# Performance work log

Measured on AMD Instinct MI355X. Metric: run time of the kernel, lower is better.

## Reference

```python
import jax, jax.numpy as jnp
import numpy as np

B, N, M = 32, 65536, 64
IMG = 640.0
POS_THR, NEG_THR = 0.5, 0.4
ALPHA, GAMMA = 0.25, 2.0
BBOX_W = 2.0
EPS = 1e-6


def setup_inputs() -> dict:
    key = jax.random.key(0)
    k1, k2, k3, k4, k5 = jax.random.split(key, 5)
    # predictions: cx, cy in [0, IMG], w, h in [8, 72], obj logit ~ N(0,1)
    cxcy = jax.random.uniform(k1, (B, N, 2), jnp.float32) * IMG
    wh = jax.random.uniform(k2, (B, N, 2), jnp.float32) * 64.0 + 8.0
    obj = jax.random.normal(k3, (B, N, 1), jnp.float32)
    predictions = jnp.concatenate([cxcy, wh, obj], axis=-1)  # [B, N, 5]
    # ground-truth boxes in xyxy, centers in [0, IMG], sizes in [10, 100]
    gcxcy = jax.random.uniform(k4, (B, M, 2), jnp.float32) * IMG
    gwh = jax.random.uniform(k5, (B, M, 2), jnp.float32) * 90.0 + 10.0
    gt_boxes = jnp.concatenate([gcxcy - gwh / 2, gcxcy + gwh / 2], axis=-1)  # [B, M, 4]
    return {"predictions": predictions, "gt_boxes": gt_boxes}


def _focal(logits, targets):
    # stable BCE-with-logits, then focal modulation
    bce = jnp.maximum(logits, 0.0) - logits * targets + jnp.log1p(jnp.exp(-jnp.abs(logits)))
    p = jax.nn.sigmoid(logits)
    p_t = jnp.where(targets == 1.0, p, 1.0 - p)
    alpha_t = jnp.where(targets == 1.0, ALPHA, 1.0 - ALPHA)
    return alpha_t * (1.0 - p_t) ** GAMMA * bce


def _pairwise_iou(pb, gb):
    # pb: [N,4] xyxy, gb: [M,4] xyxy -> [N,M]
    x1 = jnp.maximum(pb[:, None, 0], gb[None, :, 0])
    y1 = jnp.maximum(pb[:, None, 1], gb[None, :, 1])
    x2 = jnp.minimum(pb[:, None, 2], gb[None, :, 2])
    y2 = jnp.minimum(pb[:, None, 3], gb[None, :, 3])
    inter = jnp.clip(x2 - x1, 0.0) * jnp.clip(y2 - y1, 0.0)
    area_p = (pb[:, 2] - pb[:, 0]) * (pb[:, 3] - pb[:, 1])
    area_g = (gb[:, 2] - gb[:, 0]) * (gb[:, 3] - gb[:, 1])
    union = area_p[:, None] + area_g[None, :] - inter
    return inter / jnp.clip(union, EPS)


def _giou_term(pb, gb):
    # elementwise 1 - GIoU; pb, gb: [N,4]
    x1 = jnp.maximum(pb[:, 0], gb[:, 0]); y1 = jnp.maximum(pb[:, 1], gb[:, 1])
    x2 = jnp.minimum(pb[:, 2], gb[:, 2]); y2 = jnp.minimum(pb[:, 3], gb[:, 3])
    inter = jnp.clip(x2 - x1, 0.0) * jnp.clip(y2 - y1, 0.0)
    area_p = (pb[:, 2] - pb[:, 0]) * (pb[:, 3] - pb[:, 1])
    area_g = (gb[:, 2] - gb[:, 0]) * (gb[:, 3] - gb[:, 1])
    union = area_p + area_g - inter
    iou = inter / jnp.clip(union, EPS)
    ex1 = jnp.minimum(pb[:, 0], gb[:, 0]); ey1 = jnp.minimum(pb[:, 1], gb[:, 1])
    ex2 = jnp.maximum(pb[:, 2], gb[:, 2]); ey2 = jnp.maximum(pb[:, 3], gb[:, 3])
    enc = (ex2 - ex1) * (ey2 - ey1)
    giou = iou - (enc - union) / jnp.clip(enc, EPS)
    return 1.0 - giou


def _per_image(pred, gt):
    # pred: [N,5] (cx,cy,w,h,obj), gt: [M,4] xyxy
    cx, cy, w, h = pred[:, 0], pred[:, 1], pred[:, 2], pred[:, 3]
    pb = jnp.stack([cx - w / 2, cy - h / 2, cx + w / 2, cy + h / 2], axis=1)  # decode to xyxy
    obj = pred[:, 4]
    ious = _pairwise_iou(pb, gt)  # [N, M]
    best_pred_per_gt = ious.max(axis=0)              # [M]
    best_pred_idx = jnp.argmax(ious, axis=0)         # [M]
    best_gt_per_pred = ious.max(axis=1)              # [N]
    best_gt_idx = jnp.argmax(ious, axis=1)           # [N]
    # force-match each GT's best anchor if its IoU > 0.1 (scatter-max)
    pos_scatter = jnp.zeros((pred.shape[0],), jnp.int32).at[best_pred_idx].max(
        (best_pred_per_gt > 0.1).astype(jnp.int32))
    pos = (pos_scatter > 0) | (best_gt_per_pred > POS_THR)
    neg = best_gt_per_pred < NEG_THR
    valid = pos | neg
    t = pos.astype(jnp.float32)
    fl = _focal(obj, t)
    vcnt = valid.sum().astype(jnp.float32)
    cls_loss = jnp.where(vcnt > 0, (fl * valid).sum() / jnp.maximum(vcnt, 1.0), 0.0)
    matched = gt[best_gt_idx]                        # [N,4]
    gterm = _giou_term(pb, matched)                  # [N]
    pcnt = pos.sum().astype(jnp.float32)
    reg_loss = jnp.where(pcnt > 0, (gterm * pos).sum() / jnp.maximum(pcnt, 1.0), 0.0)
    return cls_loss, reg_loss, pos.sum()


def reference(predictions, gt_boxes):
    cls_b, reg_b, npos_b = jax.vmap(_per_image)(predictions, gt_boxes)
    num_pos = jnp.maximum(npos_b.sum(), 1).astype(jnp.float32)
    bsz = jnp.float32(predictions.shape[0])
    total_cls = cls_b.sum() / bsz
    total_reg = reg_b.sum() / num_pos * bsz
    return total_cls + BBOX_W * total_reg
```

## Files before the change

### kernel.cpp

```cpp
#include <hip/hip_runtime.h>

#define NB 32
#define NPRED 65536
#define NGT 64
#define BLK 256
#define SLICES 64
#define PPT 4
#define NCB 128
#define CBIN_SCALE 0.2f

#define POS_THR 0.5f
#define NEG_THR 0.4f
#define SCAT_THR 0.1f
#define EPSF 1e-6f


__device__ __forceinline__ int cbin(float x) {
    int bi = (int)(x * CBIN_SCALE);
    return max(0, min(NCB - 1, bi));
}

__device__ __forceinline__ float focal_shared(float l, bool pos) {
    float e  = expf(-fabsf(l));
    float lg = log1pf(e);
    float rp = 1.f / (1.f + e);
    float p  = (l >= 0.f) ? rp : (1.f - rp);
    if (pos) { float q = 1.f - p; return 0.25f * q * q * ((fmaxf(l, 0.f) - l) + lg); }
    return 0.75f * p * p * (fmaxf(l, 0.f) + lg);
}

__device__ __forceinline__ float giou_term(float px1, float py1, float px2, float py2,
                                           float gx1, float gy1, float gx2, float gy2) {
    float x1 = fmaxf(px1, gx1), y1 = fmaxf(py1, gy1);
    float x2 = fminf(px2, gx2), y2 = fminf(py2, gy2);
    float dx = fmaxf(__fsub_rn(x2, x1), 0.f);
    float dy = fmaxf(__fsub_rn(y2, y1), 0.f);
    float inter = __fmul_rn(dx, dy);
    float ap = __fmul_rn(__fsub_rn(px2, px1), __fsub_rn(py2, py1));
    float ag = __fmul_rn(__fsub_rn(gx2, gx1), __fsub_rn(gy2, gy1));
    float uni = __fsub_rn(__fadd_rn(ap, ag), inter);
    float iou = __fdiv_rn(inter, fmaxf(uni, EPSF));
    float ex1 = fminf(px1, gx1), ey1 = fminf(py1, gy1);
    float ex2 = fmaxf(px2, gx2), ey2 = fmaxf(py2, gy2);
    float enc = __fmul_rn(__fsub_rn(ex2, ex1), __fsub_rn(ey2, ey1));
    float giou = __fsub_rn(iou, __fdiv_rn(__fsub_rn(enc, uni), fmaxf(enc, EPSF)));
    return __fsub_rn(1.f, giou);
}


__global__ __launch_bounds__(BLK) void passA(
    const float* __restrict__ pred, const float* __restrict__ gt,
    unsigned long long* __restrict__ keys,
    double* __restrict__ S_fl, double* __restrict__ S_gt,
    int* __restrict__ vcnt, int* __restrict__ pcnt)
{
    const int b = blockIdx.y;
    const int slice = blockIdx.x;
    const int tid = threadIdx.x;
    const int lane = tid & 63;
    const int wv = tid >> 6;

    __shared__ float sgx1[NGT + 1], sgy1[NGT + 1], sgx2[NGT + 1], sgy2[NGT + 1], sgar[NGT + 1];
    __shared__ unsigned long long skey[NGT];
    __shared__ unsigned long long cums[4][NCB];
    __shared__ float rfl[BLK / 64], rgt[BLK / 64];
    __shared__ int rvp[BLK / 64];

    const unsigned base_n = (unsigned)(slice * (BLK * PPT));
    const float4* src4 = (const float4*)(pred + (size_t)b * NPRED * 5 + (size_t)base_n * 5)
                         + (size_t)tid * 5;
    float4 q0 = src4[0], q1 = src4[1], q2 = src4[2], q3 = src4[3], q4 = src4[4];

    const float4* gtb = (const float4*)(gt + (size_t)b * NGT * 4);
    float4 gmine;
    if (tid < NGT) gmine = gtb[tid];
    ((unsigned long long*)cums)[tid] = 0ULL;
    ((unsigned long long*)cums)[tid + BLK] = 0ULL;
    if (tid < NGT) {
        sgx1[tid] = gmine.x; sgy1[tid] = gmine.y;
        sgx2[tid] = gmine.z; sgy2[tid] = gmine.w;
        sgar[tid] = __fmul_rn(__fsub_rn(gmine.z, gmine.x), __fsub_rn(gmine.w, gmine.y));
        skey[tid] = 0ULL;
    } else if (tid == NGT) {
        sgx1[NGT] = 0.f; sgy1[NGT] = 0.f; sgx2[NGT] = 0.f; sgy2[NGT] = 0.f; sgar[NGT] = 0.f;
    }
    __syncthreads();

    if (tid < NGT) {
        unsigned long long bit = 1ULL << tid;
        atomicOr(&cums[0][cbin(gmine.x)], bit);
        atomicOr(&cums[1][cbin(gmine.z)], bit);
        atomicOr(&cums[2][cbin(gmine.y)], bit);
        atomicOr(&cums[3][cbin(gmine.w)], bit);
    }
    __syncthreads();

    {
        unsigned long long v0 = cums[wv][2 * lane];
        unsigned long long v1 = cums[wv][2 * lane + 1];
        unsigned long long v = v0 | v1;
        if ((wv & 1) == 0) {
            #pragma unroll
            for (int off = 1; off < 64; off <<= 1) {
                unsigned long long t = __shfl_up(v, off);
                if (lane >= off) v |= t;
            }
            unsigned long long prev = __shfl_up(v, 1);
            if (lane == 0) prev = 0ULL;
            cums[wv][2 * lane]     = prev | v0;
            cums[wv][2 * lane + 1] = v;
        } else {
            #pragma unroll
            for (int off = 1; off < 64; off <<= 1) {
                unsigned long long t = __shfl_down(v, off);
                if (lane + off < 64) v |= t;
            }
            unsigned long long nxt = __shfl_down(v, 1);
            if (lane == 63) nxt = 0ULL;
            cums[wv][2 * lane]     = v;
            cums[wv][2 * lane + 1] = v1 | nxt;
        }
    }
    __syncthreads();

    const float cxa[PPT] = {q0.x, q1.y, q2.z, q3.w};
    const float cya[PPT] = {q0.y, q1.z, q2.w, q4.x};
    const float wa [PPT] = {q0.z, q1.w, q3.x, q4.y};
    const float ha [PPT] = {q0.w, q2.x, q3.y, q4.z};
    const float oba[PPT] = {q1.x, q2.y, q3.z, q4.w};

    float acc_fl = 0.f, acc_gt = 0.f;
    int acc_vp = 0;

    #pragma unroll
    for (int i = 0; i < PPT; ++i) {
        const float px1 = __fsub_rn(cxa[i], __fmul_rn(wa[i], 0.5f));
        const float py1 = __fsub_rn(cya[i], __fmul_rn(ha[i], 0.5f));
        const float px2 = __fadd_rn(cxa[i], __fmul_rn(wa[i], 0.5f));
        const float py2 = __fadd_rn(cya[i], __fmul_rn(ha[i], 0.5f));
        const float area_p = __fmul_rn(__fsub_rn(px2, px1), __fsub_rn(py2, py1));

        unsigned long long m = (cums[1][cbin(px1)] & cums[0][cbin(px2)])
                             & (cums[3][cbin(py1)] & cums[2][cbin(py2)]);

        const unsigned n = base_n + (unsigned)(PPT * tid + i);
        const unsigned long long nkey = (unsigned long long)(~n);

        float best_iou = 0.f;
        int best_j = 0;

        int j0 = NGT, j1 = NGT;
        if (m) { j0 = __ffsll(m) - 1; m &= m - 1; }
        if (m) { j1 = __ffsll(m) - 1; m &= m - 1; }
        {
            float ax1 = sgx1[j0], ay1 = sgy1[j0], ax2 = sgx2[j0], ay2 = sgy2[j0], aga = sgar[j0];
            float bx1 = sgx1[j1], by1 = sgy1[j1], bx2 = sgx2[j1], by2 = sgy2[j1], agb = sgar[j1];
            float x1 = fmaxf(px1, ax1), y1 = fmaxf(py1, ay1);
            float x2 = fminf(px2, ax2), y2 = fminf(py2, ay2);
            float dx = fmaxf(__fsub_rn(x2, x1), 0.f);
            float dy = fmaxf(__fsub_rn(y2, y1), 0.f);
            float inter = __fmul_rn(dx, dy);
            float uni = __fsub_rn(__fadd_rn(area_p, aga), inter);
            float iou = __fdiv_rn(inter, fmaxf(uni, EPSF));
            iou = (inter > 0.f) ? iou : 0.f;
            if (iou > best_iou) { best_iou = iou; best_j = j0; }
            if (iou > SCAT_THR)
                atomicMax(&skey[j0], (((unsigned long long)__float_as_uint(iou)) << 32) | nkey);

            float X1 = fmaxf(px1, bx1), Y1 = fmaxf(py1, by1);
            float X2 = fminf(px2, bx2), Y2 = fminf(py2, by2);
            float dX = fmaxf(__fsub_rn(X2, X1), 0.f);
            float dY = fmaxf(__fsub_rn(Y2, Y1), 0.f);
            float interB = __fmul_rn(dX, dY);
            float uniB = __fsub_rn(__fadd_rn(area_p, agb), interB);
            float iouB = __fdiv_rn(interB, fmaxf(uniB, EPSF));
            iouB = (interB > 0.f) ? iouB : 0.f;
            if (iouB > best_iou) { best_iou = iouB; best_j = j1; }
            if (iouB > SCAT_THR)
                atomicMax(&skey[j1], (((unsigned long long)__float_as_uint(iouB)) << 32) | nkey);
        }

        while (m) {
            int ja = __ffsll(m) - 1; m &= m - 1;
            int jb = -1;
            if (m) { jb = __ffsll(m) - 1; m &= m - 1; }
            int jbc = (jb >= 0) ? jb : NGT;
            float ax1 = sgx1[ja], ay1 = sgy1[ja], ax2 = sgx2[ja], ay2 = sgy2[ja], aga = sgar[ja];
            float bx1 = sgx1[jbc], by1 = sgy1[jbc], bx2 = sgx2[jbc], by2 = sgy2[jbc], agb = sgar[jbc];
            {
                float x1 = fmaxf(px1, ax1), y1 = fmaxf(py1, ay1);
                float x2 = fminf(px2, ax2), y2 = fminf(py2, ay2);
                float dx = fmaxf(__fsub_rn(x2, x1), 0.f);
                float dy = fmaxf(__fsub_rn(y2, y1), 0.f);
                float inter = __fmul_rn(dx, dy);
                if (inter > 0.f) {
                    float uni = __fsub_rn(__fadd_rn(area_p, aga), inter);
                    float iou = __fdiv_rn(inter, fmaxf(uni, EPSF));
                    if (iou > best_iou) { best_iou = iou; best_j = ja; }
                    if (iou > SCAT_THR)
                        atomicMax(&skey[ja], (((unsigned long long)__float_as_uint(iou)) << 32) | nkey);
                }
            }
            if (jb >= 0) {
                float x1 = fmaxf(px1, bx1), y1 = fmaxf(py1, by1);
                float x2 = fminf(px2, bx2), y2 = fminf(py2, by2);
                float dx = fmaxf(__fsub_rn(x2, x1), 0.f);
                float dy = fmaxf(__fsub_rn(y2, y1), 0.f);
                float inter = __fmul_rn(dx, dy);
                if (inter > 0.f) {
                    float uni = __fsub_rn(__fadd_rn(area_p, agb), inter);
                    float iou = __fdiv_rn(inter, fmaxf(uni, EPSF));
                    if (iou > best_iou) { best_iou = iou; best_j = jb; }
                    if (iou > SCAT_THR)
                        atomicMax(&skey[jb], (((unsigned long long)__float_as_uint(iou)) << 32) | nkey);
                }
            }
        }

        const bool pos0   = best_iou > POS_THR;
        const bool negf   = best_iou < NEG_THR;
        const bool valid0 = pos0 || negf;
        if (valid0) acc_fl += focal_shared(oba[i], pos0);
        if (pos0) {
            acc_gt += giou_term(px1, py1, px2, py2,
                                sgx1[best_j], sgy1[best_j], sgx2[best_j], sgy2[best_j]);
        }
        acc_vp += (valid0 ? 1 : 0) | (pos0 ? 0x10000 : 0);
    }

    for (int off = 32; off; off >>= 1) {
        acc_fl += __shfl_down(acc_fl, off);
        acc_gt += __shfl_down(acc_gt, off);
        acc_vp += __shfl_down(acc_vp, off);
    }
    if (lane == 0) { rfl[wv] = acc_fl; rgt[wv] = acc_gt; rvp[wv] = acc_vp; }
    __syncthreads();
    if (tid == 0) {
        float sfl = 0.f, sgt2 = 0.f; int svp = 0;
        #pragma unroll
        for (int i = 0; i < BLK / 64; ++i) { sfl += rfl[i]; sgt2 += rgt[i]; svp += rvp[i]; }
        atomicAdd(&S_fl[b], (double)sfl);
        atomicAdd(&S_gt[b], (double)sgt2);
        atomicAdd(&vcnt[b], svp & 0xFFFF);
        atomicAdd(&pcnt[b], svp >> 16);
    }
    if (tid < NGT) {
        unsigned long long k = skey[tid];
        if (k) atomicMax(&keys[b * NGT + tid], k);
    }
}


__global__ __launch_bounds__(64) void passBC(
    const float* __restrict__ pred, const float* __restrict__ gt,
    const unsigned long long* __restrict__ keys,
    const double* __restrict__ S_fl, const double* __restrict__ S_gt,
    const int* __restrict__ vcnt, const int* __restrict__ pcnt,
    float* __restrict__ cls_b, float* __restrict__ reg_b, int* __restrict__ npos_b,
    unsigned* __restrict__ done, float* __restrict__ out)
{
    const int b = blockIdx.x;
    const int lane = threadIdx.x;

    __shared__ float4 sgt[NGT];
    __shared__ unsigned cn_list[NGT];

    const float4* gtb = (const float4*)(gt + (size_t)b * NGT * 4);
    float4 gj = gtb[lane];
    sgt[lane] = gj;

    unsigned long long key = keys[b * NGT + lane];
    float miou = __uint_as_float((unsigned)(key >> 32));
    unsigned n = ~((unsigned)(key & 0xFFFFFFFFULL));
    bool qual = miou > SCAT_THR;

    bool unique = qual;
    for (int j2 = 0; j2 < NGT; ++j2) {
        unsigned bn = __shfl(n, j2);
        int bq = __shfl((int)qual, j2);
        if (bq && j2 < lane && bn == n) unique = false;
    }
    unsigned long long mask = __ballot(unique ? 1 : 0);
    int NC = __popcll(mask);
    int slot = __popcll(mask & ((1ULL << lane) - 1ULL));
    if (unique) cn_list[slot] = n;
    __syncthreads();

    float cx = 0.f, cy = 0.f, w = 0.f, h = 0.f, obj = 0.f;
    if (lane < NC) {
        const float* p = pred + (size_t)b * NPRED * 5 + (size_t)cn_list[lane] * 5;
        cx = p[0]; cy = p[1]; w = p[2]; h = p[3]; obj = p[4];
    }
    float px1 = __fsub_rn(cx, __fmul_rn(w, 0.5f));
    float py1 = __fsub_rn(cy, __fmul_rn(h, 0.5f));
    float px2 = __fadd_rn(cx, __fmul_rn(w, 0.5f));
    float py2 = __fadd_rn(cy, __fmul_rn(h, 0.5f));
    float area_p = __fmul_rn(__fsub_rn(px2, px1), __fsub_rn(py2, py1));

    float bv = 0.f; int bj = 0;
    #pragma unroll 4
    for (int j = 0; j < NGT; ++j) {
        float4 g = sgt[j];
        float x1 = fmaxf(px1, g.x), y1 = fmaxf(py1, g.y);
        float x2 = fminf(px2, g.z), y2 = fminf(py2, g.w);
        float dx = fmaxf(__fsub_rn(x2, x1), 0.f);
        float dy = fmaxf(__fsub_rn(y2, y1), 0.f);
        float inter = __fmul_rn(dx, dy);
        if (inter > 0.f) {
            float ag = __fmul_rn(__fsub_rn(g.z, g.x), __fsub_rn(g.w, g.y));
            float uni = __fsub_rn(__fadd_rn(area_p, ag), inter);
            float iou = __fdiv_rn(inter, fmaxf(uni, EPSF));
            if (iou > bv) { bv = iou; bj = j; }
        }
    }

    double add_fl = 0.0, add_gt = 0.0;
    int add_v = 0, add_p = 0;
    if (lane < NC && !(bv > POS_THR)) {
        bool was_neg = bv < NEG_THR;
        float f1 = focal_shared(obj, true);
        float f0 = focal_shared(obj, false);
        add_fl = (double)f1 - (was_neg ? (double)f0 : 0.0);
        add_v = was_neg ? 0 : 1;
        add_p = 1;
        float4 gb = sgt[bj];
        add_gt = (double)giou_term(px1, py1, px2, py2, gb.x, gb.y, gb.z, gb.w);
    }

    for (int off = 32; off; off >>= 1) {
        add_fl += __shfl_down(add_fl, off);
        add_gt += __shfl_down(add_gt, off);
        add_v  += __shfl_down(add_v, off);
        add_p  += __shfl_down(add_p, off);
    }

    if (lane == 0) {
        double sfl = S_fl[b] + add_fl;
        double sgt2 = S_gt[b] + add_gt;
        int v = vcnt[b] + add_v;
        int pc = pcnt[b] + add_p;
        cls_b[b] = (v > 0) ? (float)(sfl / (double)(v > 1 ? v : 1)) : 0.f;
        reg_b[b] = (pc > 0) ? (float)(sgt2 / (double)(pc > 1 ? pc : 1)) : 0.f;
        npos_b[b] = pc;
    }

    __threadfence();
    unsigned t = 0;
    if (lane == 0) t = atomicAdd(done, 1u);
    t = __shfl(t, 0);
    if (t == NB - 1) {
        __threadfence();
        volatile float* vc = cls_b;
        volatile float* vr = reg_b;
        volatile int*   vn = npos_b;
        float cv = (lane < NB) ? vc[lane] : 0.f;
        float rv = (lane < NB) ? vr[lane] : 0.f;
        int   nv = (lane < NB) ? vn[lane] : 0;
        for (int off = 32; off; off >>= 1) {
            cv += __shfl_down(cv, off);
            rv += __shfl_down(rv, off);
            nv += __shfl_down(nv, off);
        }
        if (lane == 0) {
            float num_pos = fmaxf((float)nv, 1.f);
            out[0] = cv / (float)NB + 2.0f * (rv / num_pos * (float)NB);
        }
    }
}


extern "C" void kernel_launch(void* const* d_in, const int* in_sizes, int n_in,
                              void* d_out, int out_size, void* d_ws, size_t ws_size,
                              hipStream_t stream) {
    const float* pred = (const float*)d_in[0];
    const float* gt   = (const float*)d_in[1];
    float* out = (float*)d_out;

    char* ws = (char*)d_ws;
    unsigned long long* keys = (unsigned long long*)(ws + 0);
    double* S_fl   = (double*)(ws + 16384);
    double* S_gt   = (double*)(ws + 16640);
    int* vcnt      = (int*)(ws + 16896);
    int* pcnt      = (int*)(ws + 17024);
    float* cls_b   = (float*)(ws + 17152);
    float* reg_b   = (float*)(ws + 17280);
    int* npos_b    = (int*)(ws + 17408);
    unsigned* done = (unsigned*)(ws + 17536);

    hipMemsetAsync(d_ws, 0, 17664, stream);

    dim3 gridA(SLICES, NB);
    passA<<<gridA, BLK, 0, stream>>>(pred, gt, keys, S_fl, S_gt, vcnt, pcnt);
    passBC<<<NB, 64, 0, stream>>>(pred, gt, keys, S_fl, S_gt, vcnt, pcnt,
                                  cls_b, reg_b, npos_b, done, out);
}
```

Before: 119.4 us.

## Replace global atomics and memset with per-slice partials reduced in single block

passA now writes each block's partial sums and per-GT keys into dedicated per-slice slots instead of issuing double atomicAdds and 64-bit atomicMax. The memset is dropped, and the 32-block passBC with its done-counter final reduction becomes one 1024-thread block. Each wave handles two images, reduces the 64 slice partials, and does the final sum in shared memory. This removes atomic contention and the memset launch. In exchange the workspace is larger, with about 1 MB of keys to read back, and the final stage runs in a single block.

After: 154.2 us. 1.29x slower.

```diff
diff --git a/kernel.cpp b/kernel.cpp
--- a/kernel.cpp
+++ b/kernel.cpp
@@ -50,9 +50,8 @@
 
 __global__ __launch_bounds__(BLK) void passA(
     const float* __restrict__ pred, const float* __restrict__ gt,
-    unsigned long long* __restrict__ keys,
-    double* __restrict__ S_fl, double* __restrict__ S_gt,
-    int* __restrict__ vcnt, int* __restrict__ pcnt)
+    unsigned long long* __restrict__ keysP,
+    float4* __restrict__ partS)
 {
     const int b = blockIdx.y;
     const int slice = blockIdx.x;
@@ -239,123 +238,132 @@
         float sfl = 0.f, sgt2 = 0.f; int svp = 0;
         #pragma unroll
         for (int i = 0; i < BLK / 64; ++i) { sfl += rfl[i]; sgt2 += rgt[i]; svp += rvp[i]; }
-        atomicAdd(&S_fl[b], (double)sfl);
-        atomicAdd(&S_gt[b], (double)sgt2);
-        atomicAdd(&vcnt[b], svp & 0xFFFF);
-        atomicAdd(&pcnt[b], svp >> 16);
+        partS[b * SLICES + slice] = make_float4(sfl, sgt2, __int_as_float(svp), 0.f);
     }
     if (tid < NGT) {
-        unsigned long long k = skey[tid];
-        if (k) atomicMax(&keys[b * NGT + tid], k);
-    }
-}
-
-
-__global__ __launch_bounds__(64) void passBC(
+        keysP[((size_t)(b * NGT + tid)) * SLICES + slice] = skey[tid];
+    }
+}
+
+
+__global__ __launch_bounds__(1024) void passB(
     const float* __restrict__ pred, const float* __restrict__ gt,
-    const unsigned long long* __restrict__ keys,
-    const double* __restrict__ S_fl, const double* __restrict__ S_gt,
-    const int* __restrict__ vcnt, const int* __restrict__ pcnt,
-    float* __restrict__ cls_b, float* __restrict__ reg_b, int* __restrict__ npos_b,
-    unsigned* __restrict__ done, float* __restrict__ out)
+    const unsigned long long* __restrict__ keysP,
+    const float4* __restrict__ partS,
+    float* __restrict__ out)
 {
-    const int b = blockIdx.x;
-    const int lane = threadIdx.x;
-
-    __shared__ float4 sgt[NGT];
-    __shared__ unsigned cn_list[NGT];
-
-    const float4* gtb = (const float4*)(gt + (size_t)b * NGT * 4);
-    float4 gj = gtb[lane];
-    sgt[lane] = gj;
-
-    unsigned long long key = keys[b * NGT + lane];
-    float miou = __uint_as_float((unsigned)(key >> 32));
-    unsigned n = ~((unsigned)(key & 0xFFFFFFFFULL));
-    bool qual = miou > SCAT_THR;
-
-    bool unique = qual;
-    for (int j2 = 0; j2 < NGT; ++j2) {
-        unsigned bn = __shfl(n, j2);
-        int bq = __shfl((int)qual, j2);
-        if (bq && j2 < lane && bn == n) unique = false;
-    }
-    unsigned long long mask = __ballot(unique ? 1 : 0);
-    int NC = __popcll(mask);
-    int slot = __popcll(mask & ((1ULL << lane) - 1ULL));
-    if (unique) cn_list[slot] = n;
-    __syncthreads();
-
-    float cx = 0.f, cy = 0.f, w = 0.f, h = 0.f, obj = 0.f;
-    if (lane < NC) {
-        const float* p = pred + (size_t)b * NPRED * 5 + (size_t)cn_list[lane] * 5;
-        cx = p[0]; cy = p[1]; w = p[2]; h = p[3]; obj = p[4];
-    }
-    float px1 = __fsub_rn(cx, __fmul_rn(w, 0.5f));
-    float py1 = __fsub_rn(cy, __fmul_rn(h, 0.5f));
-    float px2 = __fadd_rn(cx, __fmul_rn(w, 0.5f));
-    float py2 = __fadd_rn(cy, __fmul_rn(h, 0.5f));
-    float area_p = __fmul_rn(__fsub_rn(px2, px1), __fsub_rn(py2, py1));
-
-    float bv = 0.f; int bj = 0;
-    #pragma unroll 4
-    for (int j = 0; j < NGT; ++j) {
-        float4 g = sgt[j];
-        float x1 = fmaxf(px1, g.x), y1 = fmaxf(py1, g.y);
-        float x2 = fminf(px2, g.z), y2 = fminf(py2, g.w);
-        float dx = fmaxf(__fsub_rn(x2, x1), 0.f);
-        float dy = fmaxf(__fsub_rn(y2, y1), 0.f);
-        float inter = __fmul_rn(dx, dy);
-        if (inter > 0.f) {
-            float ag = __fmul_rn(__fsub_rn(g.z, g.x), __fsub_rn(g.w, g.y));
-            float uni = __fsub_rn(__fadd_rn(area_p, ag), inter);
-            float iou = __fdiv_rn(inter, fmaxf(uni, EPSF));
-            if (iou > bv) { bv = iou; bj = j; }
-        }
-    }
-
-    double add_fl = 0.0, add_gt = 0.0;
-    int add_v = 0, add_p = 0;
-    if (lane < NC && !(bv > POS_THR)) {
-        bool was_neg = bv < NEG_THR;
-        float f1 = focal_shared(obj, true);
-        float f0 = focal_shared(obj, false);
-        add_fl = (double)f1 - (was_neg ? (double)f0 : 0.0);
-        add_v = was_neg ? 0 : 1;
-        add_p = 1;
-        float4 gb = sgt[bj];
-        add_gt = (double)giou_term(px1, py1, px2, py2, gb.x, gb.y, gb.z, gb.w);
-    }
-
-    for (int off = 32; off; off >>= 1) {
-        add_fl += __shfl_down(add_fl, off);
-        add_gt += __shfl_down(add_gt, off);
-        add_v  += __shfl_down(add_v, off);
-        add_p  += __shfl_down(add_p, off);
-    }
-
-    if (lane == 0) {
-        double sfl = S_fl[b] + add_fl;
-        double sgt2 = S_gt[b] + add_gt;
-        int v = vcnt[b] + add_v;
-        int pc = pcnt[b] + add_p;
-        cls_b[b] = (v > 0) ? (float)(sfl / (double)(v > 1 ? v : 1)) : 0.f;
-        reg_b[b] = (pc > 0) ? (float)(sgt2 / (double)(pc > 1 ? pc : 1)) : 0.f;
-        npos_b[b] = pc;
-    }
-
-    __threadfence();
-    unsigned t = 0;
-    if (lane == 0) t = atomicAdd(done, 1u);
-    t = __shfl(t, 0);
-    if (t == NB - 1) {
-        __threadfence();
-        volatile float* vc = cls_b;
-        volatile float* vr = reg_b;
-        volatile int*   vn = npos_b;
-        float cv = (lane < NB) ? vc[lane] : 0.f;
-        float rv = (lane < NB) ? vr[lane] : 0.f;
-        int   nv = (lane < NB) ? vn[lane] : 0;
+    const int tid = threadIdx.x;
+    const int lane = tid & 63;
+    const int wv = tid >> 6;
+
+    __shared__ float4 sgt[16][NGT];
+    __shared__ unsigned cn_list[16][NGT];
+    __shared__ float clsL[NB], regL[NB];
+    __shared__ int npL[NB];
+
+    #pragma unroll
+    for (int r = 0; r < 2; ++r) {
+        const int b = r * 16 + wv;
+
+        const float4* gtb = (const float4*)(gt + (size_t)b * NGT * 4);
+        float4 gj = gtb[lane];
+        sgt[wv][lane] = gj;
+
+        const unsigned long long* kp = keysP + ((size_t)(b * NGT + lane)) * SLICES;
+        const ulonglong2* kp2 = (const ulonglong2*)kp;
+        unsigned long long key = 0ULL;
+        #pragma unroll
+        for (int s = 0; s < SLICES / 2; ++s) {
+            ulonglong2 kk = kp2[s];
+            key = (kk.x > key) ? kk.x : key;
+            key = (kk.y > key) ? kk.y : key;
+        }
+
+        float miou = __uint_as_float((unsigned)(key >> 32));
+        unsigned n = ~((unsigned)(key & 0xFFFFFFFFULL));
+        bool qual = miou > SCAT_THR;
+
+        bool unique = qual;
+        for (int j2 = 0; j2 < NGT; ++j2) {
+            unsigned bn = __shfl(n, j2);
+            int bq = __shfl((int)qual, j2);
+            if (bq && j2 < lane && bn == n) unique = false;
+        }
+        unsigned long long mask = __ballot(unique ? 1 : 0);
+        int NC = __popcll(mask);
+        int slot = __popcll(mask & ((1ULL << lane) - 1ULL));
+        if (unique) cn_list[wv][slot] = n;
+
+        float cx = 0.f, cy = 0.f, w = 0.f, h = 0.f, obj = 0.f;
+        if (lane < NC) {
+            const float* p = pred + (size_t)b * NPRED * 5 + (size_t)cn_list[wv][lane] * 5;
+            cx = p[0]; cy = p[1]; w = p[2]; h = p[3]; obj = p[4];
+        }
+        float px1 = __fsub_rn(cx, __fmul_rn(w, 0.5f));
+        float py1 = __fsub_rn(cy, __fmul_rn(h, 0.5f));
+        float px2 = __fadd_rn(cx, __fmul_rn(w, 0.5f));
+        float py2 = __fadd_rn(cy, __fmul_rn(h, 0.5f));
+        float area_p = __fmul_rn(__fsub_rn(px2, px1), __fsub_rn(py2, py1));
+
+        float bv = 0.f; int bj = 0;
+        #pragma unroll 4
+        for (int j = 0; j < NGT; ++j) {
+            float4 g = sgt[wv][j];
+            float x1 = fmaxf(px1, g.x), y1 = fmaxf(py1, g.y);
+            float x2 = fminf(px2, g.z), y2 = fminf(py2, g.w);
+            float dx = fmaxf(__fsub_rn(x2, x1), 0.f);
+            float dy = fmaxf(__fsub_rn(y2, y1), 0.f);
+            float inter = __fmul_rn(dx, dy);
+            if (inter > 0.f) {
+                float ag = __fmul_rn(__fsub_rn(g.z, g.x), __fsub_rn(g.w, g.y));
+                float uni = __fsub_rn(__fadd_rn(area_p, ag), inter);
+                float iou = __fdiv_rn(inter, fmaxf(uni, EPSF));
+                if (iou > bv) { bv = iou; bj = j; }
+            }
+        }
+
+        double add_fl = 0.0, add_gt = 0.0;
+        int add_v = 0, add_p = 0;
+        if (lane < NC && !(bv > POS_THR)) {
+            bool was_neg = bv < NEG_THR;
+            float f1 = focal_shared(obj, true);
+            float f0 = focal_shared(obj, false);
+            add_fl = (double)f1 - (was_neg ? (double)f0 : 0.0);
+            add_v = was_neg ? 0 : 1;
+            add_p = 1;
+            float4 gb = sgt[wv][bj];
+            add_gt = (double)giou_term(px1, py1, px2, py2, gb.x, gb.y, gb.z, gb.w);
+        }
+
+        float4 ps = partS[b * SLICES + lane];
+        double sfl = (double)ps.x;
+        double sgt2 = (double)ps.y;
+        int vpk = __float_as_int(ps.z);
+        int sv = vpk & 0xFFFF;
+        int sp = vpk >> 16;
+
+        sfl += add_fl; sgt2 += add_gt; sv += add_v; sp += add_p;
+
+        for (int off = 32; off; off >>= 1) {
+            sfl  += __shfl_down(sfl, off);
+            sgt2 += __shfl_down(sgt2, off);
+            sv   += __shfl_down(sv, off);
+            sp   += __shfl_down(sp, off);
+        }
+
+        if (lane == 0) {
+            clsL[b] = (sv > 0) ? (float)(sfl / (double)(sv > 1 ? sv : 1)) : 0.f;
+            regL[b] = (sp > 0) ? (float)(sgt2 / (double)(sp > 1 ? sp : 1)) : 0.f;
+            npL[b] = sp;
+        }
+    }
+
+    __syncthreads();
+
+    if (wv == 0) {
+        float cv = (lane < NB) ? clsL[lane] : 0.f;
+        float rv = (lane < NB) ? regL[lane] : 0.f;
+        int   nv = (lane < NB) ? npL[lane] : 0;
         for (int off = 32; off; off >>= 1) {
             cv += __shfl_down(cv, off);
             rv += __shfl_down(rv, off);
@@ -377,20 +385,10 @@
     float* out = (float*)d_out;
 
     char* ws = (char*)d_ws;
-    unsigned long long* keys = (unsigned long long*)(ws + 0);
-    double* S_fl   = (double*)(ws + 16384);
-    double* S_gt   = (double*)(ws + 16640);
-    int* vcnt      = (int*)(ws + 16896);
-    int* pcnt      = (int*)(ws + 17024);
-    float* cls_b   = (float*)(ws + 17152);
-    float* reg_b   = (float*)(ws + 17280);
-    int* npos_b    = (int*)(ws + 17408);
-    unsigned* done = (unsigned*)(ws + 17536);
-
-    hipMemsetAsync(d_ws, 0, 17664, stream);
+    unsigned long long* keysP = (unsigned long long*)(ws + 0);
+    float4* partS = (float4*)(ws + (size_t)NB * NGT * SLICES * 8);
 
     dim3 gridA(SLICES, NB);
-    passA<<<gridA, BLK, 0, stream>>>(pred, gt, keys, S_fl, S_gt, vcnt, pcnt);
-    passBC<<<NB, 64, 0, stream>>>(pred, gt, keys, S_fl, S_gt, vcnt, pcnt,
-                                  cls_b, reg_b, npos_b, done, out);
-}
+    passA<<<gridA, BLK, 0, stream>>>(pred, gt, keysP, partS);
+    passB<<<1, 1024, 0, stream>>>(pred, gt, keysP, partS, out);
+}
```

## Replace global atomics and memset with per-slice partials reduced in second pass

Applied to the files above, without the earlier changes.

Each passA block now writes its partial sums and per-GT max keys to dedicated per-slice slots instead of issuing double/int atomicAdd and 64-bit atomicMax to shared per-image counters. passB reduces the 64 slice partials per image with a max loop and a wave reduction. The done counter is reset inside passA, which removes the hipMemsetAsync launch. This removes atomic contention and one extra stream operation, at the cost of a larger workspace and extra reads in passB. Partial sums are now kept in float per slice rather than accumulated in double.

After: 114.4 us (median of 2 runs). 4.1% less time.

```diff
diff --git a/kernel.cpp b/kernel.cpp
--- a/kernel.cpp
+++ b/kernel.cpp
@@ -50,15 +50,17 @@
 
 __global__ __launch_bounds__(BLK) void passA(
     const float* __restrict__ pred, const float* __restrict__ gt,
-    unsigned long long* __restrict__ keys,
-    double* __restrict__ S_fl, double* __restrict__ S_gt,
-    int* __restrict__ vcnt, int* __restrict__ pcnt)
+    unsigned long long* __restrict__ keysP,
+    float4* __restrict__ partS,
+    unsigned* __restrict__ done)
 {
     const int b = blockIdx.y;
     const int slice = blockIdx.x;
     const int tid = threadIdx.x;
     const int lane = tid & 63;
     const int wv = tid >> 6;
+
+    if (b == 0 && slice == 0 && tid == 0) *done = 0u;
 
     __shared__ float sgx1[NGT + 1], sgy1[NGT + 1], sgx2[NGT + 1], sgy2[NGT + 1], sgar[NGT + 1];
     __shared__ unsigned long long skey[NGT];
@@ -239,23 +241,18 @@
         float sfl = 0.f, sgt2 = 0.f; int svp = 0;
         #pragma unroll
         for (int i = 0; i < BLK / 64; ++i) { sfl += rfl[i]; sgt2 += rgt[i]; svp += rvp[i]; }
-        atomicAdd(&S_fl[b], (double)sfl);
-        atomicAdd(&S_gt[b], (double)sgt2);
-        atomicAdd(&vcnt[b], svp & 0xFFFF);
-        atomicAdd(&pcnt[b], svp >> 16);
+        partS[b * SLICES + slice] = make_float4(sfl, sgt2, __int_as_float(svp), 0.f);
     }
     if (tid < NGT) {
-        unsigned long long k = skey[tid];
-        if (k) atomicMax(&keys[b * NGT + tid], k);
-    }
-}
-
-
-__global__ __launch_bounds__(64) void passBC(
+        keysP[((size_t)b * SLICES + slice) * NGT + tid] = skey[tid];
+    }
+}
+
+
+__global__ __launch_bounds__(64) void passB(
     const float* __restrict__ pred, const float* __restrict__ gt,
-    const unsigned long long* __restrict__ keys,
-    const double* __restrict__ S_fl, const double* __restrict__ S_gt,
-    const int* __restrict__ vcnt, const int* __restrict__ pcnt,
+    const unsigned long long* __restrict__ keysP,
+    const float4* __restrict__ partS,
     float* __restrict__ cls_b, float* __restrict__ reg_b, int* __restrict__ npos_b,
     unsigned* __restrict__ done, float* __restrict__ out)
 {
@@ -269,7 +266,14 @@
     float4 gj = gtb[lane];
     sgt[lane] = gj;
 
-    unsigned long long key = keys[b * NGT + lane];
+    const unsigned long long* kp = keysP + (size_t)b * SLICES * NGT + lane;
+    unsigned long long key = 0ULL;
+    #pragma unroll 16
+    for (int s = 0; s < SLICES; ++s) {
+        unsigned long long k = kp[(size_t)s * NGT];
+        key = (k > key) ? k : key;
+    }
+
     float miou = __uint_as_float((unsigned)(key >> 32));
     unsigned n = ~((unsigned)(key & 0xFFFFFFFFULL));
     bool qual = miou > SCAT_THR;
@@ -327,21 +331,24 @@
         add_gt = (double)giou_term(px1, py1, px2, py2, gb.x, gb.y, gb.z, gb.w);
     }
 
+    float4 ps = partS[b * SLICES + lane];
+    double sfl = (double)ps.x + add_fl;
+    double sgt2 = (double)ps.y + add_gt;
+    int vpk = __float_as_int(ps.z);
+    int sv = (vpk & 0xFFFF) + add_v;
+    int sp = (vpk >> 16) + add_p;
+
     for (int off = 32; off; off >>= 1) {
-        add_fl += __shfl_down(add_fl, off);
-        add_gt += __shfl_down(add_gt, off);
-        add_v  += __shfl_down(add_v, off);
-        add_p  += __shfl_down(add_p, off);
+        sfl  += __shfl_down(sfl, off);
+        sgt2 += __shfl_down(sgt2, off);
+        sv   += __shfl_down(sv, off);
+        sp   += __shfl_down(sp, off);
     }
 
     if (lane == 0) {
-        double sfl = S_fl[b] + add_fl;
-        double sgt2 = S_gt[b] + add_gt;
-        int v = vcnt[b] + add_v;
-        int pc = pcnt[b] + add_p;
-        cls_b[b] = (v > 0) ? (float)(sfl / (double)(v > 1 ? v : 1)) : 0.f;
-        reg_b[b] = (pc > 0) ? (float)(sgt2 / (double)(pc > 1 ? pc : 1)) : 0.f;
-        npos_b[b] = pc;
+        cls_b[b] = (sv > 0) ? (float)(sfl / (double)(sv > 1 ? sv : 1)) : 0.f;
+        reg_b[b] = (sp > 0) ? (float)(sgt2 / (double)(sp > 1 ? sp : 1)) : 0.f;
+        npos_b[b] = sp;
     }
 
     __threadfence();
@@ -377,20 +384,16 @@
     float* out = (float*)d_out;
 
     char* ws = (char*)d_ws;
-    unsigned long long* keys = (unsigned long long*)(ws + 0);
-    double* S_fl   = (double*)(ws + 16384);
-    double* S_gt   = (double*)(ws + 16640);
-    int* vcnt      = (int*)(ws + 16896);
-    int* pcnt      = (int*)(ws + 17024);
-    float* cls_b   = (float*)(ws + 17152);
-    float* reg_b   = (float*)(ws + 17280);
-    int* npos_b    = (int*)(ws + 17408);
-    unsigned* done = (unsigned*)(ws + 17536);
-
-    hipMemsetAsync(d_ws, 0, 17664, stream);
+    unsigned long long* keysP = (unsigned long long*)(ws + 0);
+    float4* partS = (float4*)(ws + (size_t)NB * SLICES * NGT * 8);
+    char* tail = ws + (size_t)NB * SLICES * NGT * 8 + (size_t)NB * SLICES * 16;
+    float* cls_b   = (float*)(tail);
+    float* reg_b   = (float*)(tail + 128);
+    int* npos_b    = (int*)(tail + 256);
+    unsigned* done = (unsigned*)(tail + 384);
 
     dim3 gridA(SLICES, NB);
-    passA<<<gridA, BLK, 0, stream>>>(pred, gt, keys, S_fl, S_gt, vcnt, pcnt);
-    passBC<<<NB, 64, 0, stream>>>(pred, gt, keys, S_fl, S_gt, vcnt, pcnt,
-                                  cls_b, reg_b, npos_b, done, out);
-}
+    passA<<<gridA, BLK, 0, stream>>>(pred, gt, keysP, partS, done);
+    passB<<<NB, 64, 0, stream>>>(pred, gt, keysP, partS,
+                                 cls_b, reg_b, npos_b, done, out);
+}
```
